# Performance work log

Measured on AMD Instinct MI355X. Metric: run time of the kernel, lower is better.

The kernel has to match this reference:

```python
import jax, jax.numpy as jnp
import numpy as np

B, S, E, H = 4, 2048, 1024, 16
HD = E // H  # head dim = 64
EPS = 1e-5


def layernorm(x, g, b):
    mu = jnp.mean(x, axis=-1, keepdims=True)
    var = jnp.var(x, axis=-1, keepdims=True)
    return (x - mu) * jax.lax.rsqrt(var + EPS) * g + b


def setup_inputs() -> dict:
    key = jax.random.key(0)
    ks = jax.random.split(key, 10)
    std = 1.0 / np.sqrt(E)
    def lin(k):
        kw, kb = jax.random.split(k)
        return (jax.random.uniform(kw, (E, E), jnp.float32, -std, std),
                jax.random.uniform(kb, (E,), jnp.float32, -std, std))
    wq, bq = lin(ks[0]); wk, bk = lin(ks[1]); wv, bv = lin(ks[2]); wp, bp = lin(ks[3])
    ones = jnp.ones((E,), jnp.float32); zeros = jnp.zeros((E,), jnp.float32)
    x = jax.random.normal(ks[4], (B, S, E), jnp.float32)
    return {
        'x': x,
        'wq': wq, 'bq': bq, 'wk': wk, 'bk': bk, 'wv': wv, 'bv': bv, 'wp': wp, 'bp': bp,
        'g_q': ones, 'be_q': zeros, 'g_k': ones, 'be_k': zeros,
        'g_v': ones, 'be_v': zeros, 'g_p': ones, 'be_p': zeros,
    }


def reference(x, wq, bq, wk, bk, wv, bv, wp, bp,
              g_q, be_q, g_k, be_k, g_v, be_v, g_p, be_p):
    def heads(t):  # [B,S,E] -> [B,H,S,HD]
        return t.reshape(B, S, H, HD).transpose(0, 2, 1, 3)

    Q = heads(layernorm(x @ wq.T + bq, g_q, be_q))
    K = heads(layernorm(x @ wk.T + bk, g_k, be_k))
    V = heads(layernorm(x @ wv.T + bv, g_v, be_v))

    scores = jnp.einsum('bhqd,bhkd->bhqk', Q, K) * (HD ** -0.5)
    causal = jnp.tril(jnp.ones((S, S), bool))  # [S,S]
    scores = jnp.where(causal[None, None], scores, -jnp.inf)
    attn = jax.nn.softmax(scores, axis=-1)
    out = jnp.einsum('bhqk,bhkd->bhqd', attn, V)
    out = out.transpose(0, 2, 1, 3).reshape(B, S, E)
    out = layernorm(out @ wp.T + bp, g_p, be_p)
    return out, V
```

## Files before the change

kernel.cpp:

```cpp
#include <hip/hip_runtime.h>
#include <hip/hip_bf16.h>

typedef unsigned short u16;
typedef __attribute__((ext_vector_type(8))) short short8;
typedef __attribute__((ext_vector_type(4))) float f32x4;

__device__ __forceinline__ float b2f(u16 u){
    unsigned v = ((unsigned)u) << 16; float f; __builtin_memcpy(&f, &v, 4); return f;
}
__device__ __forceinline__ u16 f2b(float f){
    unsigned v; __builtin_memcpy(&v, &f, 4);
    v += 0x7fffu + ((v >> 16) & 1u);
    return (u16)(v >> 16);
}
__device__ __forceinline__ unsigned pk2(float lo, float hi){
    unsigned a, b; __builtin_memcpy(&a, &lo, 4); __builtin_memcpy(&b, &hi, 4);
    return __builtin_amdgcn_perm(b + 0x8000u, a + 0x8000u, 0x07060302u);
}

__device__ __forceinline__ void gload16(const void* g, void* l){
    __builtin_amdgcn_global_load_lds((const __attribute__((address_space(1))) unsigned int*)g,
                                     (__attribute__((address_space(3))) unsigned int*)l, 16, 0, 0);
}

__device__ __forceinline__ int swz(int row, int col){
    return row * 64 + (col ^ ((row & 7) << 3));
}

__global__ void cvtall_k(const float* __restrict__ x,
                         const float* __restrict__ wq, const float* __restrict__ wk,
                         const float* __restrict__ wv, const float* __restrict__ wp,
                         u16* __restrict__ xb, u16* __restrict__ wb)
{
    const int blk = blockIdx.x;
    const float* src; u16* dst;
    if (blk < 8192) {
        src = x + (size_t)blk * 1024; dst = xb + (size_t)blk * 1024;
    } else {
        const int m = (blk - 8192) >> 10, r = (blk - 8192) & 1023;
        const float* w = (m == 0) ? wq : (m == 1) ? wk : (m == 2) ? wv : wp;
        src = w + (size_t)r * 1024; dst = wb + ((size_t)m << 20) + (size_t)r * 1024;
    }
    const int i = threadIdx.x * 4;
    float4 v = *(const float4*)&src[i];
    ushort4 o;
    o.x = f2b(v.x); o.y = f2b(v.y); o.z = f2b(v.z); o.w = f2b(v.w);
    *(ushort4*)&dst[i] = o;
}

__global__ __launch_bounds__(256, 2)
void gemm3_k(const u16* __restrict__ A, const u16* __restrict__ Wb,
             const float* __restrict__ b0, const float* __restrict__ b1,
             const float* __restrict__ b2,
             u16* __restrict__ C0, u16* __restrict__ C1, u16* __restrict__ C2)
{
    __shared__ u16 As[128 * 32];
    __shared__ u16 Bs[128 * 32];
    const int K = 1024, N = 1024;
    const int mat = blockIdx.y >> 3;
    const int n0  = (blockIdx.y & 7) * 128;
    const u16* W = Wb + ((size_t)mat << 20);
    const float* bias = (mat == 0) ? b0 : (mat == 1) ? b1 : b2;
    u16* C = (mat == 0) ? C0 : (mat == 1) ? C1 : C2;

    const int tid  = threadIdx.x;
    const int wave = tid >> 6, lane = tid & 63;
    const int lg = lane >> 4, lr = lane & 15;
    const int m0 = blockIdx.x * 128;
    const int wm = (wave >> 1) * 64, wn = (wave & 1) * 64;

    const u16* aG = A + (size_t)(m0 + (tid >> 2)) * K + (tid & 3) * 8;
    const u16* bG = W + (size_t)(n0 + (tid >> 2)) * K + (tid & 3) * 8;
    char* asBase = (char*)As + wave * 1024;
    char* bsBase = (char*)Bs + wave * 1024;
    const size_t rstep = (size_t)64 * K;

    f32x4 acc[4][4] = {};

    for (int kt = 0; kt < K; kt += 32) {
        gload16(aG + kt,         asBase);
        gload16(aG + kt + rstep, asBase + 4096);
        gload16(bG + kt,         bsBase);
        gload16(bG + kt + rstep, bsBase + 4096);
        __syncthreads();

        short8 a[4], b[4];
#pragma unroll
        for (int i = 0; i < 4; ++i) a[i] = *(const short8*)&As[(wm + i*16 + lr)*32 + lg*8];
#pragma unroll
        for (int j = 0; j < 4; ++j) b[j] = *(const short8*)&Bs[(wn + j*16 + lr)*32 + lg*8];
        __builtin_amdgcn_s_setprio(1);
#pragma unroll
        for (int i = 0; i < 4; ++i)
#pragma unroll
            for (int j = 0; j < 4; ++j)
                acc[i][j] = __builtin_amdgcn_mfma_f32_16x16x32_bf16(a[i], b[j], acc[i][j], 0, 0, 0);
        __builtin_amdgcn_s_setprio(0);
        __syncthreads();
    }

#pragma unroll
    for (int j = 0; j < 4; ++j) {
        const int cn = n0 + wn + j*16 + lr;
        const float bv = bias[cn];
#pragma unroll
        for (int i = 0; i < 4; ++i) {
            const int cm = m0 + wm + i*16 + lg*4;
#pragma unroll
            for (int r = 0; r < 4; ++r)
                C[(size_t)(cm + r) * N + cn] = f2b(acc[i][j][r] + bv);
        }
    }
}

__global__ __launch_bounds__(256, 2)
void gemm_k(const u16* __restrict__ A, const u16* __restrict__ W,
            const float* __restrict__ bias, u16* __restrict__ C,
            int M, int N, int K)
{
    __shared__ u16 As[128 * 32];
    __shared__ u16 Bs[128 * 32];
    const int tid  = threadIdx.x;
    const int wave = tid >> 6, lane = tid & 63;
    const int lg = lane >> 4, lr = lane & 15;
    const int m0 = blockIdx.x * 128, n0 = blockIdx.y * 128;
    const int wm = (wave >> 1) * 64, wn = (wave & 1) * 64;

    const u16* aG = A + (size_t)(m0 + (tid >> 2)) * K + (tid & 3) * 8;
    const u16* bG = W + (size_t)(n0 + (tid >> 2)) * K + (tid & 3) * 8;
    char* asBase = (char*)As + wave * 1024;
    char* bsBase = (char*)Bs + wave * 1024;
    const size_t rstep = (size_t)64 * K;

    f32x4 acc[4][4] = {};

    for (int kt = 0; kt < K; kt += 32) {
        gload16(aG + kt,         asBase);
        gload16(aG + kt + rstep, asBase + 4096);
        gload16(bG + kt,         bsBase);
        gload16(bG + kt + rstep, bsBase + 4096);
        __syncthreads();

        short8 a[4], b[4];
#pragma unroll
        for (int i = 0; i < 4; ++i) a[i] = *(const short8*)&As[(wm + i*16 + lr)*32 + lg*8];
#pragma unroll
        for (int j = 0; j < 4; ++j) b[j] = *(const short8*)&Bs[(wn + j*16 + lr)*32 + lg*8];
        __builtin_amdgcn_s_setprio(1);
#pragma unroll
        for (int i = 0; i < 4; ++i)
#pragma unroll
            for (int j = 0; j < 4; ++j)
                acc[i][j] = __builtin_amdgcn_mfma_f32_16x16x32_bf16(a[i], b[j], acc[i][j], 0, 0, 0);
        __builtin_amdgcn_s_setprio(0);
        __syncthreads();
    }

#pragma unroll
    for (int j = 0; j < 4; ++j) {
        const int cn = n0 + wn + j*16 + lr;
        const float bv = bias[cn];
#pragma unroll
        for (int i = 0; i < 4; ++i) {
            const int cm = m0 + wm + i*16 + lg*4;
#pragma unroll
            for (int r = 0; r < 4; ++r)
                C[(size_t)(cm + r) * N + cn] = f2b(acc[i][j][r] + bv);
        }
    }
}

__global__ void ln3_k(u16* D0, u16* D1, const u16* __restrict__ Sv,
                      const float* __restrict__ g_q, const float* __restrict__ be_q,
                      const float* __restrict__ g_k, const float* __restrict__ be_k,
                      const float* __restrict__ g_v, const float* __restrict__ be_v,
                      float* __restrict__ Vf)
{
    __shared__ float red[8];
    const int which = blockIdx.y;
    const u16* src = (which == 0) ? D0 : (which == 1) ? D1 : Sv;
    const float* g  = (which == 0) ? g_q  : (which == 1) ? g_k  : g_v;
    const float* be = (which == 0) ? be_q : (which == 1) ? be_k : be_v;
    const float scale = (which == 0) ? 0.125f * 1.4426950408889634f : 1.0f;

    const int row = blockIdx.x;
    const int tid = threadIdx.x;
    const int lane = tid & 63, wave = tid >> 6;
    ushort4 v = *(const ushort4*)&src[(size_t)row * 1024 + tid * 4];
    float f[4] = { b2f(v.x), b2f(v.y), b2f(v.z), b2f(v.w) };
    float s  = f[0] + f[1] + f[2] + f[3];
    float ss = f[0]*f[0] + f[1]*f[1] + f[2]*f[2] + f[3]*f[3];
#pragma unroll
    for (int off = 32; off; off >>= 1) { s += __shfl_down(s, off); ss += __shfl_down(ss, off); }
    if (lane == 0) { red[wave] = s; red[4 + wave] = ss; }
    __syncthreads();
    s  = red[0] + red[1] + red[2] + red[3];
    ss = red[4] + red[5] + red[6] + red[7];
    const float mean = s * (1.0f / 1024.0f);
    const float var  = fmaxf(ss * (1.0f / 1024.0f) - mean * mean, 0.0f);
    const float rs   = rsqrtf(var + 1e-5f);
    float o[4];
#pragma unroll
    for (int k = 0; k < 4; ++k) {
        const int e = tid * 4 + k;
        o[k] = ((f[k] - mean) * rs * g[e] + be[e]) * scale;
    }
    if (which == 2) {
        const int b = row >> 11, sIdx = row & 2047;
        const int h = tid >> 4, hd = (tid * 4) & 63;
        float4 ov = { o[0], o[1], o[2], o[3] };
        *(float4*)&Vf[(((size_t)(b * 16 + h) * 2048 + sIdx) << 6) + hd] = ov;
    } else {
        u16* dst = (which == 0) ? D0 : D1;
        ushort4 ov; ov.x = f2b(o[0]); ov.y = f2b(o[1]); ov.z = f2b(o[2]); ov.w = f2b(o[3]);
        *(ushort4*)&dst[(size_t)row * 1024 + tid * 4] = ov;
    }
}

__global__ void lnf_k(const u16* __restrict__ src, const float* __restrict__ g,
                      const float* __restrict__ be, float* __restrict__ dst)
{
    __shared__ float red[8];
    const int row = blockIdx.x;
    const int tid = threadIdx.x;
    const int lane = tid & 63, wave = tid >> 6;
    ushort4 v = *(const ushort4*)&src[(size_t)row * 1024 + tid * 4];
    float f[4] = { b2f(v.x), b2f(v.y), b2f(v.z), b2f(v.w) };
    float s  = f[0] + f[1] + f[2] + f[3];
    float ss = f[0]*f[0] + f[1]*f[1] + f[2]*f[2] + f[3]*f[3];
#pragma unroll
    for (int off = 32; off; off >>= 1) { s += __shfl_down(s, off); ss += __shfl_down(ss, off); }
    if (lane == 0) { red[wave] = s; red[4 + wave] = ss; }
    __syncthreads();
    s  = red[0] + red[1] + red[2] + red[3];
    ss = red[4] + red[5] + red[6] + red[7];
    const float mean = s * (1.0f / 1024.0f);
    const float var  = fmaxf(ss * (1.0f / 1024.0f) - mean * mean, 0.0f);
    const float rs   = rsqrtf(var + 1e-5f);
    float4 ov;
    ov.x = (f[0] - mean) * rs * g[tid*4+0] + be[tid*4+0];
    ov.y = (f[1] - mean) * rs * g[tid*4+1] + be[tid*4+1];
    ov.z = (f[2] - mean) * rs * g[tid*4+2] + be[tid*4+2];
    ov.w = (f[3] - mean) * rs * g[tid*4+3] + be[tid*4+3];
    *(float4*)&dst[(size_t)row * 1024 + tid * 4] = ov;
}

__global__ void vtr_k(const float* __restrict__ Vf, u16* __restrict__ Vt)
{
    __shared__ float T[64 * 65];
    const int bh = blockIdx.x >> 5, st = blockIdx.x & 31;
    const int tid = threadIdx.x;
    const float* src = Vf + (size_t)bh * 2048 * 64 + (size_t)st * 64 * 64;
#pragma unroll
    for (int it = 0; it < 4; ++it) {
        const int fid = tid + it * 256;
        const int r = fid >> 4, c4 = fid & 15;
        float4 v = *(const float4*)&src[r * 64 + c4 * 4];
        T[r * 65 + c4*4 + 0] = v.x;
        T[r * 65 + c4*4 + 1] = v.y;
        T[r * 65 + c4*4 + 2] = v.z;
        T[r * 65 + c4*4 + 3] = v.w;
    }
    __syncthreads();
    u16* dst = Vt + (size_t)bh * 64 * 2048 + (size_t)st * 64;
#pragma unroll
    for (int it = 0; it < 2; ++it) {
        const int oid = tid + it * 256;
        const int hd = oid >> 3, ch = oid & 7;
        u16 tmp[8];
#pragma unroll
        for (int j = 0; j < 8; ++j) tmp[j] = f2b(T[(ch * 8 + j) * 65 + hd]);
        const int base = 32 * (ch >> 2) + 4 * ((ch >> 1) & 1);
        const int p0 = base + 8 * ((2 * ch + 0) & 3);
        const int p1 = base + 8 * ((2 * ch + 1) & 3);
        ushort4 lo = { tmp[0], tmp[1], tmp[2], tmp[3] };
        ushort4 hi = { tmp[4], tmp[5], tmp[6], tmp[7] };
        *(ushort4*)&dst[(size_t)hd * 2048 + p0] = lo;
        *(ushort4*)&dst[(size_t)hd * 2048 + p1] = hi;
    }
}

__global__ __launch_bounds__(512, 4)
void attn_k(const u16* __restrict__ Qf, const u16* __restrict__ Kf,
            const u16* __restrict__ Vt, u16* __restrict__ O)
{
    __shared__ u16 Lds[16384];
    const int lin = (int)blockIdx.x + (int)blockIdx.y * 16;
    const int xcd = lin & 7, idx = lin >> 3;
    const int bh  = xcd * 8 + (idx & 7);
    const int qt  = 15 - (idx >> 3);
    const int b = bh >> 4, h = bh & 15;
    const int tid = threadIdx.x, wave = tid >> 6, lane = tid & 63;
    const int lg = lane >> 4, lr = lane & 15;
    const u16* Qbh = Qf + ((size_t)b * 2048) * 1024 + h * 64;
    const u16* Kbh = Kf + ((size_t)b * 2048) * 1024 + h * 64;
    const u16* Vbh = Vt + (size_t)bh * 64 * 2048;
    u16* Obh = O + ((size_t)b * 2048) * 1024 + h * 64;

    const int q0w  = qt * 128 + wave * 16;
    const int qrow = q0w + lr;
    const short8 qf0 = *(const short8*)&Qbh[(size_t)qrow * 1024 + lg * 8];
    const short8 qf1 = *(const short8*)&Qbh[(size_t)qrow * 1024 + 32 + lg * 8];

    const int nkv    = 2 * qt + 2;
    const int diagkv = q0w >> 6;

    const int kro0 = swz(lr, lg * 8) * 2;
    const int kro1 = swz(lr, 32 + lg * 8) * 2;
    const int vro0 = 8192 + kro0;
    const int vro1 = 8192 + kro1;
    const char* ldsB = (const char*)Lds;

    const int sr = tid >> 3;
    const int sc8 = ((tid & 7) ^ (sr & 7)) * 8;
    const u16* kg = Kbh + (size_t)sr * 1024 + sc8;
    const u16* vg = Vbh + (size_t)sr * 2048 + sc8;
    const int stKo = wave * 1024;

    f32x4 oacc[4] = {};
    float l_r = 0.f, m_r = -1e30f;

    gload16(kg, (char*)Lds + stKo);
    gload16(vg, (char*)Lds + 8192 + stKo);
    kg += 65536; vg += 64;
    __syncthreads();

    int rbuf = 0, sbuf = 16384;
    for (int kv = 0; kv < nkv; ++kv) {
        if (kv + 1 < nkv) {
            gload16(kg, (char*)Lds + sbuf + stKo);
            gload16(vg, (char*)Lds + sbuf + 8192 + stKo);
            kg += 65536; vg += 64;
        }

        if (kv <= diagkv) {
            const char* kp0 = ldsB + (rbuf + kro0);
            const char* kp1 = ldsB + (rbuf + kro1);

            f32x4 sacc[4];
#pragma unroll
            for (int c = 0; c < 4; ++c) {
                const short8 k0 = *(const short8*)(kp0 + c * 2048);
                const short8 k1 = *(const short8*)(kp1 + c * 2048);
                f32x4 z = { 0.f, 0.f, 0.f, 0.f };
                __builtin_amdgcn_s_setprio(1);
                z = __builtin_amdgcn_mfma_f32_16x16x32_bf16(k0, qf0, z, 0, 0, 0);
                z = __builtin_amdgcn_mfma_f32_16x16x32_bf16(k1, qf1, z, 0, 0, 0);
                __builtin_amdgcn_s_setprio(0);
                sacc[c] = z;
            }

            if (kv == diagkv) {
                const int kbase = kv * 64 + 4 * lg;
#pragma unroll
                for (int c = 0; c < 4; ++c)
#pragma unroll
                    for (int r = 0; r < 4; ++r)
                        if (kbase + c * 16 + r > qrow) sacc[c][r] = -1e30f;
            }

            float t0 = fmaxf(fmaxf(sacc[0][0], sacc[0][1]), sacc[0][2]);
            float t1 = fmaxf(fmaxf(sacc[0][3], sacc[1][0]), sacc[1][1]);
            float t2 = fmaxf(fmaxf(sacc[1][2], sacc[1][3]), sacc[2][0]);
            float t3 = fmaxf(fmaxf(sacc[2][1], sacc[2][2]), sacc[2][3]);
            float t4 = fmaxf(fmaxf(sacc[3][0], sacc[3][1]), sacc[3][2]);
            float mx = fmaxf(fmaxf(fmaxf(t0, t1), fmaxf(t2, t3)),
                             fmaxf(t4, sacc[3][3]));
            mx = fmaxf(mx, __shfl_xor(mx, 16));
            mx = fmaxf(mx, __shfl_xor(mx, 32));

            const float df = mx - m_r;
            if (__any(df > 8.0f)) {
                const float mn = (df > 8.0f) ? mx : m_r;
                const float al = exp2f(m_r - mn);
                m_r = mn;
                l_r *= al;
#pragma unroll
                for (int r = 0; r < 4; ++r) {
                    const float alo = __shfl(al, 4 * lg + r);
#pragma unroll
                    for (int c2 = 0; c2 < 4; ++c2) oacc[c2][r] *= alo;
                }
            }

#pragma unroll
            for (int c = 0; c < 4; ++c)
#pragma unroll
                for (int r = 0; r < 4; ++r) sacc[c][r] = exp2f(sacc[c][r] - m_r);
            {
                float s0 = (sacc[0][0] + sacc[0][1]) + (sacc[0][2] + sacc[0][3]);
                float s1 = (sacc[1][0] + sacc[1][1]) + (sacc[1][2] + sacc[1][3]);
                float s2 = (sacc[2][0] + sacc[2][1]) + (sacc[2][2] + sacc[2][3]);
                float s3 = (sacc[3][0] + sacc[3][1]) + (sacc[3][2] + sacc[3][3]);
                float ts = (s0 + s1) + (s2 + s3);
                ts += __shfl_xor(ts, 16);
                ts += __shfl_xor(ts, 32);
                l_r += ts;
            }

            const char* vp0 = ldsB + (rbuf + vro0);
            const char* vp1 = ldsB + (rbuf + vro1);
#pragma unroll
            for (int m2 = 0; m2 < 2; ++m2) {
                union { unsigned w[4]; short8 v; } pa;
                pa.w[0] = pk2(sacc[2*m2][0],   sacc[2*m2][1]);
                pa.w[1] = pk2(sacc[2*m2][2],   sacc[2*m2][3]);
                pa.w[2] = pk2(sacc[2*m2+1][0], sacc[2*m2+1][1]);
                pa.w[3] = pk2(sacc[2*m2+1][2], sacc[2*m2+1][3]);
                const char* vp = m2 ? vp1 : vp0;
                __builtin_amdgcn_s_setprio(1);
#pragma unroll
                for (int c2 = 0; c2 < 4; ++c2) {
                    const short8 vb = *(const short8*)(vp + c2 * 2048);
                    oacc[c2] = __builtin_amdgcn_mfma_f32_16x16x32_bf16(pa.v, vb, oacc[c2], 0, 0, 0);
                }
                __builtin_amdgcn_s_setprio(0);
            }
        }
        rbuf ^= 16384; sbuf ^= 16384;
        __syncthreads();
    }

    float lo[4];
#pragma unroll
    for (int r = 0; r < 4; ++r) lo[r] = 1.0f / __shfl(l_r, 4 * lg + r);
#pragma unroll
    for (int c2 = 0; c2 < 4; ++c2)
#pragma unroll
        for (int r = 0; r < 4; ++r) {
            const float ov = oacc[c2][r] * lo[r];
            Obh[(size_t)(q0w + 4 * lg + r) * 1024 + c2 * 16 + lr] = f2b(ov);
        }
}

extern "C" void kernel_launch(void* const* d_in, const int* in_sizes, int n_in,
                              void* d_out, int out_size, void* d_ws, size_t ws_size,
                              hipStream_t stream)
{
    (void)in_sizes; (void)n_in; (void)out_size; (void)ws_size;
    const float* x   = (const float*)d_in[0];
    const float* wq  = (const float*)d_in[1];  const float* bq   = (const float*)d_in[2];
    const float* wk  = (const float*)d_in[3];  const float* bk   = (const float*)d_in[4];
    const float* wv  = (const float*)d_in[5];  const float* bv   = (const float*)d_in[6];
    const float* wp  = (const float*)d_in[7];  const float* bp   = (const float*)d_in[8];
    const float* g_q = (const float*)d_in[9];  const float* be_q = (const float*)d_in[10];
    const float* g_k = (const float*)d_in[11]; const float* be_k = (const float*)d_in[12];
    const float* g_v = (const float*)d_in[13]; const float* be_v = (const float*)d_in[14];
    const float* g_p = (const float*)d_in[15]; const float* be_p = (const float*)d_in[16];

    float* outF = (float*)d_out;
    float* Vf   = outF + 8388608;
    u16* D0 = (u16*)d_out;
    u16* D1 = (u16*)d_out + 8388608;
    u16* xb = (u16*)d_out + 16777216;
    char* ws = (char*)d_ws;
    u16* S0  = (u16*)ws;
    u16* wb  = (u16*)(ws + 16777216);
    u16* wpb = wb + 3145728;

    const dim3 bb(256);
    cvtall_k<<<dim3(12288), bb, 0, stream>>>(x, wq, wk, wv, wp, xb, wb);

    gemm3_k<<<dim3(64, 24), bb, 0, stream>>>(xb, wb, bq, bk, bv, D0, D1, S0);
    ln3_k<<<dim3(8192, 3), bb, 0, stream>>>(D0, D1, S0, g_q, be_q, g_k, be_k, g_v, be_v, Vf);
    vtr_k<<<dim3(2048), bb, 0, stream>>>(Vf, S0);
    attn_k<<<dim3(16, 64), dim3(512), 0, stream>>>(D0, D1, S0, D0);
    gemm_k<<<dim3(64, 8), bb, 0, stream>>>(D0, wpb, bp, S0, 8192, 1024, 1024);
    lnf_k<<<dim3(8192), bb, 0, stream>>>(S0, g_p, be_p, outF);
}
```

Before: 208.9 us.

## Deepen GEMM K-tile with swizzled LDS and triple-buffer attention KV

Both GEMM kernels now stage a 64-wide K slice per iteration into an XOR-swizzled LDS layout. This halves the number of barrier round-trips and is meant to reduce LDS bank conflicts on the fragment reads. The attention kernel moves from double to triple buffering of K/V tiles, using explicit vmcnt waits and raw barriers so that two tiles are in flight at once. The cost is more LDS per block: 32KB for the GEMMs and 48KB for attention. That may lower attention occupancy below the requested 4 blocks per CU. The code also relies on a swz helper that is not added here and must already exist elsewhere.

```diff
diff --git a/kernel.cpp b/kernel.cpp
--- a/kernel.cpp
+++ b/kernel.cpp
@@ -4,6 +4,9 @@
 typedef unsigned short u16;
 typedef __attribute__((ext_vector_type(8))) short short8;
 typedef __attribute__((ext_vector_type(4))) float f32x4;
+
+#define VMCNT2 asm volatile("s_waitcnt vmcnt(2)" ::: "memory")
+#define VMCNT0 asm volatile("s_waitcnt vmcnt(0)" ::: "memory")
 
 __device__ __forceinline__ float b2f(u16 u){
     unsigned v = ((unsigned)u) << 16; float f; __builtin_memcpy(&f, &v, 4); return f;
@@ -54,8 +57,8 @@
              const float* __restrict__ b2,
              u16* __restrict__ C0, u16* __restrict__ C1, u16* __restrict__ C2)
 {
-    __shared__ u16 As[128 * 32];
-    __shared__ u16 Bs[128 * 32];
+    __shared__ u16 As[128 * 64];
+    __shared__ u16 Bs[128 * 64];
     const int K = 1024, N = 1024;
     const int mat = blockIdx.y >> 3;
     const int n0  = (blockIdx.y & 7) * 128;
@@ -69,33 +72,39 @@
     const int m0 = blockIdx.x * 128;
     const int wm = (wave >> 1) * 64, wn = (wave & 1) * 64;
 
-    const u16* aG = A + (size_t)(m0 + (tid >> 2)) * K + (tid & 3) * 8;
-    const u16* bG = W + (size_t)(n0 + (tid >> 2)) * K + (tid & 3) * 8;
+    const int srow = tid >> 3;
+    const int sc8  = ((tid & 7) ^ (srow & 7)) * 8;
+    const u16* aG = A + (size_t)(m0 + srow) * K + sc8;
+    const u16* bG = W + (size_t)(n0 + srow) * K + sc8;
     char* asBase = (char*)As + wave * 1024;
     char* bsBase = (char*)Bs + wave * 1024;
-    const size_t rstep = (size_t)64 * K;
+    const size_t rstep = (size_t)32 * K;
 
     f32x4 acc[4][4] = {};
 
-    for (int kt = 0; kt < K; kt += 32) {
-        gload16(aG + kt,         asBase);
-        gload16(aG + kt + rstep, asBase + 4096);
-        gload16(bG + kt,         bsBase);
-        gload16(bG + kt + rstep, bsBase + 4096);
+    for (int kt = 0; kt < K; kt += 64) {
+#pragma unroll
+        for (int i = 0; i < 4; ++i) {
+            gload16(aG + kt + i * rstep, asBase + i * 4096);
+            gload16(bG + kt + i * rstep, bsBase + i * 4096);
+        }
         __syncthreads();
 
-        short8 a[4], b[4];
-#pragma unroll
-        for (int i = 0; i < 4; ++i) a[i] = *(const short8*)&As[(wm + i*16 + lr)*32 + lg*8];
-#pragma unroll
-        for (int j = 0; j < 4; ++j) b[j] = *(const short8*)&Bs[(wn + j*16 + lr)*32 + lg*8];
-        __builtin_amdgcn_s_setprio(1);
-#pragma unroll
-        for (int i = 0; i < 4; ++i)
-#pragma unroll
-            for (int j = 0; j < 4; ++j)
-                acc[i][j] = __builtin_amdgcn_mfma_f32_16x16x32_bf16(a[i], b[j], acc[i][j], 0, 0, 0);
-        __builtin_amdgcn_s_setprio(0);
+#pragma unroll
+        for (int s = 0; s < 2; ++s) {
+            short8 a[4], b[4];
+#pragma unroll
+            for (int i = 0; i < 4; ++i) a[i] = *(const short8*)&As[swz(wm + i*16 + lr, s*32 + lg*8)];
+#pragma unroll
+            for (int j = 0; j < 4; ++j) b[j] = *(const short8*)&Bs[swz(wn + j*16 + lr, s*32 + lg*8)];
+            __builtin_amdgcn_s_setprio(1);
+#pragma unroll
+            for (int i = 0; i < 4; ++i)
+#pragma unroll
+                for (int j = 0; j < 4; ++j)
+                    acc[i][j] = __builtin_amdgcn_mfma_f32_16x16x32_bf16(a[i], b[j], acc[i][j], 0, 0, 0);
+            __builtin_amdgcn_s_setprio(0);
+        }
         __syncthreads();
     }
 
@@ -118,41 +127,47 @@
             const float* __restrict__ bias, u16* __restrict__ C,
             int M, int N, int K)
 {
-    __shared__ u16 As[128 * 32];
-    __shared__ u16 Bs[128 * 32];
+    __shared__ u16 As[128 * 64];
+    __shared__ u16 Bs[128 * 64];
     const int tid  = threadIdx.x;
     const int wave = tid >> 6, lane = tid & 63;
     const int lg = lane >> 4, lr = lane & 15;
     const int m0 = blockIdx.x * 128, n0 = blockIdx.y * 128;
     const int wm = (wave >> 1) * 64, wn = (wave & 1) * 64;
 
-    const u16* aG = A + (size_t)(m0 + (tid >> 2)) * K + (tid & 3) * 8;
-    const u16* bG = W + (size_t)(n0 + (tid >> 2)) * K + (tid & 3) * 8;
+    const int srow = tid >> 3;
+    const int sc8  = ((tid & 7) ^ (srow & 7)) * 8;
+    const u16* aG = A + (size_t)(m0 + srow) * K + sc8;
+    const u16* bG = W + (size_t)(n0 + srow) * K + sc8;
     char* asBase = (char*)As + wave * 1024;
     char* bsBase = (char*)Bs + wave * 1024;
-    const size_t rstep = (size_t)64 * K;
+    const size_t rstep = (size_t)32 * K;
 
     f32x4 acc[4][4] = {};
 
-    for (int kt = 0; kt < K; kt += 32) {
-        gload16(aG + kt,         asBase);
-        gload16(aG + kt + rstep, asBase + 4096);
-        gload16(bG + kt,         bsBase);
-        gload16(bG + kt + rstep, bsBase + 4096);
+    for (int kt = 0; kt < K; kt += 64) {
+#pragma unroll
+        for (int i = 0; i < 4; ++i) {
+            gload16(aG + kt + i * rstep, asBase + i * 4096);
+            gload16(bG + kt + i * rstep, bsBase + i * 4096);
+        }
         __syncthreads();
 
-        short8 a[4], b[4];
-#pragma unroll
-        for (int i = 0; i < 4; ++i) a[i] = *(const short8*)&As[(wm + i*16 + lr)*32 + lg*8];
-#pragma unroll
-        for (int j = 0; j < 4; ++j) b[j] = *(const short8*)&Bs[(wn + j*16 + lr)*32 + lg*8];
-        __builtin_amdgcn_s_setprio(1);
-#pragma unroll
-        for (int i = 0; i < 4; ++i)
-#pragma unroll
-            for (int j = 0; j < 4; ++j)
-                acc[i][j] = __builtin_amdgcn_mfma_f32_16x16x32_bf16(a[i], b[j], acc[i][j], 0, 0, 0);
-        __builtin_amdgcn_s_setprio(0);
+#pragma unroll
+        for (int s = 0; s < 2; ++s) {
+            short8 a[4], b[4];
+#pragma unroll
+            for (int i = 0; i < 4; ++i) a[i] = *(const short8*)&As[swz(wm + i*16 + lr, s*32 + lg*8)];
+#pragma unroll
+            for (int j = 0; j < 4; ++j) b[j] = *(const short8*)&Bs[swz(wn + j*16 + lr, s*32 + lg*8)];
+            __builtin_amdgcn_s_setprio(1);
+#pragma unroll
+            for (int i = 0; i < 4; ++i)
+#pragma unroll
+                for (int j = 0; j < 4; ++j)
+                    acc[i][j] = __builtin_amdgcn_mfma_f32_16x16x32_bf16(a[i], b[j], acc[i][j], 0, 0, 0);
+            __builtin_amdgcn_s_setprio(0);
+        }
         __syncthreads();
     }
 
@@ -284,7 +299,7 @@
 void attn_k(const u16* __restrict__ Qf, const u16* __restrict__ Kf,
             const u16* __restrict__ Vt, u16* __restrict__ O)
 {
-    __shared__ u16 Lds[16384];
+    __shared__ u16 Lds[24576];
     const int lin = (int)blockIdx.x + (int)blockIdx.y * 16;
     const int xcd = lin & 7, idx = lin >> 3;
     const int bh  = xcd * 8 + (idx & 7);
@@ -320,35 +335,40 @@
     f32x4 oacc[4] = {};
     float l_r = 0.f, m_r = -1e30f;
 
-    gload16(kg, (char*)Lds + stKo);
-    gload16(vg, (char*)Lds + 8192 + stKo);
-    kg += 65536; vg += 64;
-    __syncthreads();
-
-    int rbuf = 0, sbuf = 16384;
+    gload16(kg,          (char*)Lds + stKo);
+    gload16(vg,          (char*)Lds + 8192 + stKo);
+    gload16(kg + 65536,  (char*)Lds + 16384 + stKo);
+    gload16(vg + 64,     (char*)Lds + 16384 + 8192 + stKo);
+    kg += 131072; vg += 128;
+    VMCNT2;
+    __builtin_amdgcn_s_barrier();
+
+    int ro = 0;
     for (int kv = 0; kv < nkv; ++kv) {
-        if (kv + 1 < nkv) {
-            gload16(kg, (char*)Lds + sbuf + stKo);
-            gload16(vg, (char*)Lds + sbuf + 8192 + stKo);
+        const bool doStage = (kv + 2 < nkv);
+        if (doStage) {
+            int so = ro + 32768; if (so >= 49152) so -= 49152;
+            gload16(kg, (char*)Lds + so + stKo);
+            gload16(vg, (char*)Lds + so + 8192 + stKo);
             kg += 65536; vg += 64;
         }
 
         if (kv <= diagkv) {
-            const char* kp0 = ldsB + (rbuf + kro0);
-            const char* kp1 = ldsB + (rbuf + kro1);
+            const char* kp0 = ldsB + (ro + kro0);
+            const char* kp1 = ldsB + (ro + kro1);
 
             f32x4 sacc[4];
+            __builtin_amdgcn_s_setprio(1);
 #pragma unroll
             for (int c = 0; c < 4; ++c) {
                 const short8 k0 = *(const short8*)(kp0 + c * 2048);
                 const short8 k1 = *(const short8*)(kp1 + c * 2048);
                 f32x4 z = { 0.f, 0.f, 0.f, 0.f };
-                __builtin_amdgcn_s_setprio(1);
                 z = __builtin_amdgcn_mfma_f32_16x16x32_bf16(k0, qf0, z, 0, 0, 0);
                 z = __builtin_amdgcn_mfma_f32_16x16x32_bf16(k1, qf1, z, 0, 0, 0);
-                __builtin_amdgcn_s_setprio(0);
                 sacc[c] = z;
             }
+            __builtin_amdgcn_s_setprio(0);
 
             if (kv == diagkv) {
                 const int kbase = kv * 64 + 4 * lg;
@@ -398,8 +418,8 @@
                 l_r += ts;
             }
 
-            const char* vp0 = ldsB + (rbuf + vro0);
-            const char* vp1 = ldsB + (rbuf + vro1);
+            const char* vp0 = ldsB + (ro + vro0);
+            const char* vp1 = ldsB + (ro + vro1);
 #pragma unroll
             for (int m2 = 0; m2 < 2; ++m2) {
                 union { unsigned w[4]; short8 v; } pa;
@@ -417,8 +437,13 @@
                 __builtin_amdgcn_s_setprio(0);
             }
         }
-        rbuf ^= 16384; sbuf ^= 16384;
-        __syncthreads();
+
+        if (kv + 1 < nkv) {
+            if (doStage) { VMCNT2; }
+            else        { VMCNT0; }
+            __builtin_amdgcn_s_barrier();
+        }
+        ro += 16384; if (ro == 49152) ro = 0;
     }
 
     float lo[4];
```

Result: faster. 194.1 us (-7.1%).
